# Optimization experiments

Hardware: AMD Instinct MI355X
Metric: run time of the kernel (lower is better)

Reference implementation:

```python
import jax, jax.numpy as jnp
import numpy as np
from jax import lax

# mamba-130m-hf config
N_LAYERS = 24
D_MODEL = 768
D_INNER = 1536   # expand=2
D_STATE = 16
DT_RANK = 48     # ceil(768/16)
D_CONV = 4
VOCAB = 50280
ENC_DIM = 256
EPS = 1e-5
SEQ, BATCH = 512, 2  # input is (SEQ, BATCH, ENC_DIM); permute -> mamba batch=BATCH, seq=SEQ


def setup_inputs() -> dict:
    key = jax.random.key(0)
    ks = jax.random.split(key, 12)
    f = jnp.float32
    def rn(k, shape, scale=0.02):
        return (jax.random.normal(k, shape) * scale).astype(f)
    x = jax.random.normal(ks[0], (SEQ, BATCH, ENC_DIM), dtype=f)
    W_et = rn(ks[1], (D_MODEL, ENC_DIM))
    b_et = jnp.zeros((D_MODEL,), f)
    in_proj_w = rn(ks[2], (N_LAYERS, 2 * D_INNER, D_MODEL))
    conv_w = rn(ks[3], (N_LAYERS, D_INNER, D_CONV), 0.1)
    conv_b = jnp.zeros((N_LAYERS, D_INNER), f)
    x_proj_w = rn(ks[4], (N_LAYERS, DT_RANK + 2 * D_STATE, D_INNER))
    dt_proj_w = rn(ks[5], (N_LAYERS, D_INNER, DT_RANK), 0.1)
    # bias init so softplus(bias) lands in [1e-3, 1e-1] (standard mamba dt init)
    dt_init = jnp.exp(jax.random.uniform(ks[6], (N_LAYERS, D_INNER), minval=jnp.log(1e-3), maxval=jnp.log(1e-1)))
    dt_proj_b = jnp.log(jnp.expm1(dt_init)).astype(f)
    A_log = jnp.log(jnp.broadcast_to(jnp.arange(1, D_STATE + 1, dtype=f), (N_LAYERS, D_INNER, D_STATE))) * jnp.ones((1,), f)
    D = jnp.ones((N_LAYERS, D_INNER), f)
    out_proj_w = rn(ks[7], (N_LAYERS, D_MODEL, D_INNER))
    norm_w = jnp.ones((N_LAYERS, D_MODEL), f)
    final_norm_w = jnp.ones((D_MODEL,), f)
    embed = rn(ks[8], (VOCAB, D_MODEL))
    return {"x": x, "W_et": W_et, "b_et": b_et, "in_proj_w": in_proj_w, "conv_w": conv_w,
            "conv_b": conv_b, "x_proj_w": x_proj_w, "dt_proj_w": dt_proj_w, "dt_proj_b": dt_proj_b,
            "A_log": A_log, "D": D, "out_proj_w": out_proj_w, "norm_w": norm_w,
            "final_norm_w": final_norm_w, "embed": embed}


def rmsnorm(x, w):
    return x * lax.rsqrt(jnp.mean(x * x, axis=-1, keepdims=True) + EPS) * w


def mamba_layer(h, p):
    in_w, cw, cb, xw, dtw, dtb, Al, Dv, ow, nw = p
    hn = rmsnorm(h, nw)
    xz = hn @ in_w.T                       # (B,T,2*D_INNER)
    xi, z = jnp.split(xz, 2, axis=-1)
    # depthwise causal conv over time
    xc = lax.conv_general_dilated(xi.transpose(0, 2, 1), cw[:, None, :], (1,),
                                  [(D_CONV - 1, 0)], dimension_numbers=("NCH", "OIH", "NCH"),
                                  feature_group_count=D_INNER)
    xc = jax.nn.silu(xc + cb[None, :, None]).transpose(0, 2, 1)   # (B,T,D_INNER)
    proj = xc @ xw.T                                              # (B,T,DT_RANK+2*D_STATE)
    dt = jax.nn.softplus(proj[..., :DT_RANK] @ dtw.T + dtb)       # (B,T,D_INNER)
    Bm = proj[..., DT_RANK:DT_RANK + D_STATE]                     # (B,T,S)
    Cm = proj[..., DT_RANK + D_STATE:]                            # (B,T,S)
    A = -jnp.exp(Al)                                              # (D_INNER,S)
    dA = jnp.exp(dt[..., None] * A)                               # (B,T,D,S)
    dBx = dt[..., None] * Bm[:, :, None, :] * xc[..., None]       # (B,T,D,S)

    def step(hst, inp):
        a, bx, c = inp
        hst = a * hst + bx
        return hst, jnp.einsum("bds,bs->bd", hst, c)

    h0 = jnp.zeros(dA.shape[:1] + dA.shape[2:], dA.dtype)
    _, ys = lax.scan(step, h0, (dA.transpose(1, 0, 2, 3), dBx.transpose(1, 0, 2, 3), Cm.transpose(1, 0, 2)))
    y = ys.transpose(1, 0, 2) + Dv * xc
    y = y * jax.nn.silu(z)
    return h + y @ ow.T


def reference(x, W_et, b_et, in_proj_w, conv_w, conv_b, x_proj_w, dt_proj_w, dt_proj_b,
              A_log, D, out_proj_w, norm_w, final_norm_w, embed):
    h = (x @ W_et.T + b_et).transpose(1, 0, 2)   # permute(1,0,2): (B,T,D_MODEL)

    def body(hc, p):
        return mamba_layer(hc, p), None

    h, _ = lax.scan(body, h, (in_proj_w, conv_w, conv_b, x_proj_w, dt_proj_w,
                              dt_proj_b, A_log, D, out_proj_w, norm_w))
    h = rmsnorm(h, final_norm_w)
    return h @ embed.T                            # tied lm_head logits (B,T,VOCAB)
```

## Files before the change

### kernel.cpp

```cpp
#include <hip/hip_runtime.h>
#include <math.h>

#define N_LAYERS 24
#define D_MODEL 768
#define D_INNER 1536
#define D_STATE 16
#define DT_RANK 48
#define D_CONV 4
#define VOCAB 50280
#define ENC_DIM 256
#define SEQ 512
#define BATCH 2
#define NTOK (SEQ*BATCH)
#define XZ_DIM (2*D_INNER)
#define PROJ_DIM (DT_RANK + 2*D_STATE)
#define DTW_PAD 64
#define IN_SPLIT 2
#define XP_SPLIT 8
#define OP_SPLIT 4

typedef __attribute__((ext_vector_type(8))) short bf16x8;
typedef __attribute__((ext_vector_type(4))) float f32x4;

__device__ __forceinline__ float sigmoidf_(float x) { return 1.f / (1.f + __expf(-x)); }
__device__ __forceinline__ float softplusf_(float x) {
    return fmaxf(x, 0.f) + log1pf(__expf(-fabsf(x)));
}
__device__ __forceinline__ short f2bf(float f) {
    unsigned u = __float_as_uint(f);
    unsigned r = (u + 0x7FFFu + ((u >> 16) & 1u)) >> 16;
    return (short)r;
}
__device__ __forceinline__ float bf2f(short s) {
    return __uint_as_float(((unsigned)(unsigned short)s) << 16);
}
__device__ __forceinline__ void load_lds16(const void* g, void* l) {
    __builtin_amdgcn_global_load_lds((const __attribute__((address_space(1))) void*)g,
                                     (__attribute__((address_space(3))) void*)l, 16, 0, 0);
}

__global__ __launch_bounds__(256) void cvt_k(const float* __restrict__ s,
                                             short* __restrict__ d, int n) {
    int stride = gridDim.x * 256 * 4;
    for (int i = (blockIdx.x * 256 + threadIdx.x) * 4; i + 3 < n; i += stride) {
        float4 f = *(const float4*)(s + i);
        short4 o; o.x = f2bf(f.x); o.y = f2bf(f.y); o.z = f2bf(f.z); o.w = f2bf(f.w);
        *(short4*)(d + i) = o;
    }
}

__global__ __launch_bounds__(256) void pad_dtw_k(const float* __restrict__ src,
                                                 short* __restrict__ dst) {
    int i = blockIdx.x * 256 + threadIdx.x;
    if (i >= N_LAYERS * D_INNER * DTW_PAD) return;
    int k = i & (DTW_PAD - 1);
    int rest = i >> 6;
    dst[i] = (k < DT_RANK) ? f2bf(src[(size_t)rest * DT_RANK + k]) : (short)0;
}

__global__ __launch_bounds__(256) void transpose_x_k(const float* __restrict__ x,
                                                     float* __restrict__ xt) {
    int i = blockIdx.x * 256 + threadIdx.x;
    if (i >= SEQ * BATCH * ENC_DIM) return;
    int e = i % ENC_DIM;
    int b = (i / ENC_DIM) % BATCH;
    int l = i / (ENC_DIM * BATCH);
    xt[((size_t)(b * SEQ + l)) * ENC_DIM + e] = x[i];
}
__global__ __launch_bounds__(256) void transpose_x_bf_k(const float* __restrict__ x,
                                                        short* __restrict__ xt) {
    int i = blockIdx.x * 256 + threadIdx.x;
    if (i >= SEQ * BATCH * ENC_DIM) return;
    int e = i % ENC_DIM;
    int b = (i / ENC_DIM) % BATCH;
    int l = i / (ENC_DIM * BATCH);
    xt[((size_t)(b * SEQ + l)) * ENC_DIM + e] = f2bf(x[i]);
}

__device__ __forceinline__ float rms_scale(const float* r, int tid) {
    float s = 0.f;
    for (int i = tid; i < D_MODEL; i += 256) { float v = r[i]; s += v * v; }
    for (int o = 32; o > 0; o >>= 1) s += __shfl_down(s, o);
    __shared__ float wsum[4];
    if ((tid & 63) == 0) wsum[tid >> 6] = s;
    __syncthreads();
    float tot = wsum[0] + wsum[1] + wsum[2] + wsum[3];
    return rsqrtf(tot / (float)D_MODEL + 1e-5f);
}
__global__ __launch_bounds__(256) void rmsnorm_k(const float* __restrict__ in,
                                                 const float* __restrict__ w,
                                                 float* __restrict__ out) {
    int row = blockIdx.x;
    const float* r = in + (size_t)row * D_MODEL;
    float sc = rms_scale(r, threadIdx.x);
    for (int i = threadIdx.x; i < D_MODEL; i += 256)
        out[(size_t)row * D_MODEL + i] = r[i] * sc * w[i];
}
__global__ __launch_bounds__(256) void rmsnorm_bf_k(const float* __restrict__ in,
                                                    const float* __restrict__ w,
                                                    short* __restrict__ out) {
    int row = blockIdx.x;
    const float* r = in + (size_t)row * D_MODEL;
    float sc = rms_scale(r, threadIdx.x);
    for (int i = threadIdx.x; i < D_MODEL; i += 256)
        out[(size_t)row * D_MODEL + i] = f2bf(r[i] * sc * w[i]);
}

template<int MODE, int BM, int DEPTH>
__global__ __launch_bounds__(256)
void gemm_p2(const short* __restrict__ A, const short* __restrict__ B,
             const float* __restrict__ bias, float* __restrict__ C,
             short* __restrict__ Cb,
             int M, int N, int K, int ldaE, int ldbE, int ldc, int ldcb)
{
    constexpr int NBUF = DEPTH + 1;
    constexpr int MI = BM / 32;
    constexpr int AELEM = 4 * BM;
    constexpr int BELEM = 4 * 128;
    constexpr int LA = AELEM / 256;
    constexpr int LB = BELEM / 256;
    constexpr int L = LA + LB;
    __shared__ short lA[NBUF][AELEM * 8];
    __shared__ short lB[NBUF][BELEM * 8];

    const int nx = gridDim.x;
    int lin = blockIdx.y * nx + blockIdx.x;
    const int nwg = nx * gridDim.y;
    if ((nwg & 7) == 0) { const int cpx = nwg >> 3; lin = (lin & 7) * cpx + (lin >> 3); }
    const int bm = (lin % nx) * BM;
    const int bn = (lin / nx) * 128;
    const int koff = blockIdx.z * K;

    const int t = threadIdx.x;
    const int wave = t >> 6;
    const int wm = (wave >> 1) * (BM / 2), wn = (wave & 1) * 64;
    const int l15 = t & 15, l4 = (t & 63) >> 4;

    f32x4 acc[MI][4] = {};
    const int nkt = K / 32;

    auto stage = [&](int buf, int kt) {
        const int k0 = koff + kt * 32;
        #pragma unroll
        for (int u = 0; u < LA; ++u) {
            const int idx = t + u * 256;
            const int kg = idx / BM;
            const int row = idx % BM;
            load_lds16(A + (size_t)(bm + row) * ldaE + k0 + kg * 8,
                       &lA[buf][(wave * 64 + u * 256) * 8]);
        }
        #pragma unroll
        for (int u = 0; u < LB; ++u) {
            const int idx = t + u * 256;
            const int kg = idx >> 7;
            const int row = idx & 127;
            int brow = bn + row; if (brow >= N) brow = 0;
            load_lds16(B + (size_t)brow * ldbE + k0 + kg * 8,
                       &lB[buf][(wave * 64 + u * 256) * 8]);
        }
    };

    #pragma unroll
    for (int p = 0; p < DEPTH; ++p)
        if (p < nkt) stage(p, p);

    for (int kt = 0; kt < nkt; ++kt) {
        const int rem = nkt - 1 - kt;
        const int ahead = rem < (DEPTH - 1) ? rem : (DEPTH - 1);
        if (ahead == 2) {
            if constexpr (L == 3) asm volatile("s_waitcnt vmcnt(6)" ::: "memory");
            else                  asm volatile("s_waitcnt vmcnt(8)" ::: "memory");
        } else if (ahead == 1) {
            if constexpr (L == 3) asm volatile("s_waitcnt vmcnt(3)" ::: "memory");
            else                  asm volatile("s_waitcnt vmcnt(4)" ::: "memory");
        } else {
            asm volatile("s_waitcnt vmcnt(0)" ::: "memory");
        }
        __builtin_amdgcn_s_barrier();
        __builtin_amdgcn_sched_barrier(0);
        if (kt + DEPTH < nkt) stage((kt + DEPTH) % NBUF, kt + DEPTH);
        const int cbuf = kt % NBUF;
        const short* bA = lA[cbuf];
        const short* bB = lB[cbuf];
        bf16x8 af[MI], bfr[4];
        #pragma unroll
        for (int i = 0; i < MI; ++i)
            af[i] = *(const bf16x8*)&bA[(l4 * BM + wm + i * 16 + l15) * 8];
        #pragma unroll
        for (int j = 0; j < 4; ++j)
            bfr[j] = *(const bf16x8*)&bB[(l4 * 128 + wn + j * 16 + l15) * 8];
        #pragma unroll
        for (int i = 0; i < MI; ++i)
            #pragma unroll
            for (int j = 0; j < 4; ++j)
                acc[i][j] = __builtin_amdgcn_mfma_f32_16x16x32_bf16(
                    af[i], bfr[j], acc[i][j], 0, 0, 0);
    }

    float* Cp = (MODE == 5) ? C + (size_t)blockIdx.z * M * ldc : C;
    #pragma unroll
    for (int i = 0; i < MI; ++i) {
        #pragma unroll
        for (int r = 0; r < 4; ++r) {
            const int row = bm + wm + i * 16 + l4 * 4 + r;
            #pragma unroll
            for (int j = 0; j < 4; ++j) {
                const int col = bn + wn + j * 16 + l15;
                if (col < N) {
                    float v = acc[i][j][r];
                    if (MODE == 6) {
                        Cb[(size_t)row * ldcb + col] = f2bf(softplusf_(v + bias[col]));
                    } else {
                        if (MODE == 1) v += bias[col];
                        if (MODE == 2) v = softplusf_(v + bias[col]);
                        if (MODE == 3) v += C[(size_t)row * ldc + col];
                        Cp[(size_t)row * ldc + col] = v;
                        if (MODE == 4) Cb[(size_t)row * ldcb + col] = f2bf(v);
                    }
                }
            }
        }
    }
}

__global__ __launch_bounds__(256) void reduce_conv_k(const float* __restrict__ part,
                                                     const float* __restrict__ cw,
                                                     const float* __restrict__ cb,
                                                     short* __restrict__ xcb,
                                                     short* __restrict__ zb) {
    int idx = blockIdx.x * 256 + threadIdx.x;
    if (idx >= NTOK * XZ_DIM) return;
    int d3 = idx % XZ_DIM;
    int m  = idx / XZ_DIM;
    if (d3 < D_INNER) {
        int l = m % SEQ;
        float acc = cb[d3];
        #pragma unroll
        for (int j = 0; j < D_CONV; ++j) {
            int ll = l - (D_CONV - 1) + j;
            if (ll >= 0) {
                int mm = m - (D_CONV - 1) + j;
                float v = part[(size_t)mm * XZ_DIM + d3]
                        + part[(size_t)(NTOK + mm) * XZ_DIM + d3];
                acc = fmaf(cw[d3 * D_CONV + j], v, acc);
            }
        }
        float v = acc * sigmoidf_(acc);
        xcb[(size_t)m * D_INNER + d3] = f2bf(v);
    } else {
        int d = d3 - D_INNER;
        float z = part[(size_t)m * XZ_DIM + d3]
                + part[(size_t)(NTOK + m) * XZ_DIM + d3];
        zb[(size_t)m * D_INNER + d] = f2bf(z);
    }
}

__global__ __launch_bounds__(256) void reduce_xp_k(const float* __restrict__ part,
                                                   float* __restrict__ proj,
                                                   short* __restrict__ projb) {
    const int n4 = NTOK * PROJ_DIM / 4;
    int i = blockIdx.x * 256 + threadIdx.x;
    if (i >= n4) return;
    float4 s = ((const float4*)part)[i];
    #pragma unroll
    for (int p = 1; p < XP_SPLIT; ++p) {
        float4 v = ((const float4*)part)[i + p * n4];
        s.x += v.x; s.y += v.y; s.z += v.z; s.w += v.w;
    }
    ((float4*)proj)[i] = s;
    short4 o; o.x = f2bf(s.x); o.y = f2bf(s.y); o.z = f2bf(s.z); o.w = f2bf(s.w);
    ((short4*)projb)[i] = o;
}

__global__ __launch_bounds__(256) void reduce_rms_k(const float* __restrict__ part,
                                                    float* __restrict__ h,
                                                    const float* __restrict__ w,
                                                    short* __restrict__ hnb) {
    const int row = blockIdx.x;
    const int i = threadIdx.x;
    float4 s = make_float4(0.f, 0.f, 0.f, 0.f);
    if (i < 192) {
        s = ((const float4*)h)[row * 192 + i];
        #pragma unroll
        for (int p = 0; p < OP_SPLIT; ++p) {
            float4 v = ((const float4*)part)[((size_t)p * NTOK + row) * 192 + i];
            s.x += v.x; s.y += v.y; s.z += v.z; s.w += v.w;
        }
        ((float4*)h)[row * 192 + i] = s;
    }
    float ss = s.x * s.x + s.y * s.y + s.z * s.z + s.w * s.w;
    for (int o = 32; o > 0; o >>= 1) ss += __shfl_down(ss, o);
    __shared__ float wsum[4];
    if ((i & 63) == 0) wsum[i >> 6] = ss;
    __syncthreads();
    float tot = wsum[0] + wsum[1] + wsum[2] + wsum[3];
    float sc = rsqrtf(tot / (float)D_MODEL + 1e-5f);
    if (i < 192) {
        float4 w4 = ((const float4*)w)[i];
        short4 o4;
        o4.x = f2bf(s.x * sc * w4.x); o4.y = f2bf(s.y * sc * w4.y);
        o4.z = f2bf(s.z * sc * w4.z); o4.w = f2bf(s.w * sc * w4.w);
        ((short4*)hnb)[row * 192 + i] = o4;
    }
}

template<int MODE>
__global__ __launch_bounds__(256)
void gemm_bf16(const float* __restrict__ A, const float* __restrict__ B,
               const float* __restrict__ bias, float* __restrict__ C,
               int M, int N, int K, int lda, int ldb, int ldc)
{
    __shared__ short lA[4 * 128 * 8];
    __shared__ short lB[4 * 128 * 8];
    const int bm = blockIdx.x * 128;
    const int bn = blockIdx.y * 128;
    const int t = threadIdx.x;
    const int wave = t >> 6, lane = t & 63;
    const int wm = (wave >> 1) * 64, wn = (wave & 1) * 64;
    const int l15 = lane & 15, l4 = lane >> 4;
    const int row2 = t >> 1;
    const int khalf = (t & 1) * 16;
    const int kgbase = khalf >> 3;
    f32x4 acc[4][4] = {};
    const int nkt = (K + 31) / 32;
    for (int kt = 0; kt < nkt; ++kt) {
        const int k0 = kt * 32 + khalf;
        {
            short v[16];
            const float* src = A + (size_t)(bm + row2) * lda + k0;
            if (k0 + 16 <= K) {
                #pragma unroll
                for (int j = 0; j < 16; j += 4) {
                    float4 f = *(const float4*)(src + j);
                    v[j+0]=f2bf(f.x); v[j+1]=f2bf(f.y); v[j+2]=f2bf(f.z); v[j+3]=f2bf(f.w);
                }
            } else {
                #pragma unroll
                for (int j = 0; j < 16; ++j)
                    v[j] = (k0 + j < K) ? f2bf(src[j]) : (short)0;
            }
            short* dst = &lA[(kgbase * 128 + row2) * 8];
            *(bf16x8*)dst = *(const bf16x8*)&v[0];
            *(bf16x8*)(dst + 128 * 8) = *(const bf16x8*)&v[8];
        }
        {
            short v[16];
            const int nrow = bn + row2;
            if (nrow < N) {
                const float* src = B + (size_t)nrow * ldb + k0;
                if (k0 + 16 <= K) {
                    #pragma unroll
                    for (int j = 0; j < 16; j += 4) {
                        float4 f = *(const float4*)(src + j);
                        v[j+0]=f2bf(f.x); v[j+1]=f2bf(f.y); v[j+2]=f2bf(f.z); v[j+3]=f2bf(f.w);
                    }
                } else {
                    #pragma unroll
                    for (int j = 0; j < 16; ++j)
                        v[j] = (k0 + j < K) ? f2bf(src[j]) : (short)0;
                }
            } else {
                #pragma unroll
                for (int j = 0; j < 16; ++j) v[j] = 0;
            }
            short* dst = &lB[(kgbase * 128 + row2) * 8];
            *(bf16x8*)dst = *(const bf16x8*)&v[0];
            *(bf16x8*)(dst + 128 * 8) = *(const bf16x8*)&v[8];
        }
        __syncthreads();
        bf16x8 af[4], bfr[4];
        #pragma unroll
        for (int i = 0; i < 4; ++i)
            af[i] = *(const bf16x8*)&lA[(l4 * 128 + wm + i * 16 + l15) * 8];
        #pragma unroll
        for (int j = 0; j < 4; ++j)
            bfr[j] = *(const bf16x8*)&lB[(l4 * 128 + wn + j * 16 + l15) * 8];
        #pragma unroll
        for (int i = 0; i < 4; ++i)
            #pragma unroll
            for (int j = 0; j < 4; ++j)
                acc[i][j] = __builtin_amdgcn_mfma_f32_16x16x32_bf16(
                    af[i], bfr[j], acc[i][j], 0, 0, 0);
        __syncthreads();
    }
    #pragma unroll
    for (int i = 0; i < 4; ++i) {
        #pragma unroll
        for (int r = 0; r < 4; ++r) {
            const int row = bm + wm + i * 16 + l4 * 4 + r;
            #pragma unroll
            for (int j = 0; j < 4; ++j) {
                const int col = bn + wn + j * 16 + l15;
                if (col < N) {
                    float v = acc[i][j][r];
                    if (MODE == 1) v += bias[col];
                    if (MODE == 2) v = softplusf_(v + bias[col]);
                    if (MODE == 3) v += C[(size_t)row * ldc + col];
                    C[(size_t)row * ldc + col] = v;
                }
            }
        }
    }
}

template<int DUAL>
__global__ __launch_bounds__(256) void conv_silu_k(const float* __restrict__ xz,
                                                   const float* __restrict__ cw,
                                                   const float* __restrict__ cb,
                                                   float* __restrict__ xc,
                                                   short* __restrict__ xcb) {
    int idx = blockIdx.x * 256 + threadIdx.x;
    if (idx >= NTOK * D_INNER) return;
    int d = idx % D_INNER;
    int m = idx / D_INNER;
    int l = m % SEQ;
    float acc = cb[d];
    #pragma unroll
    for (int j = 0; j < D_CONV; ++j) {
        int ll = l - (D_CONV - 1) + j;
        if (ll >= 0)
            acc = fmaf(cw[d * D_CONV + j],
                       xz[(size_t)(m - (D_CONV - 1) + j) * XZ_DIM + d], acc);
    }
    float v = acc * sigmoidf_(acc);
    xc[(size_t)m * D_INNER + d] = v;
    if (DUAL) xcb[(size_t)m * D_INNER + d] = f2bf(v);
}

#define SCAN_DW 16
#define SCAN_NC 32
#define SCAN_CL (SEQ / SCAN_NC)
template<int BF>
__global__ __launch_bounds__(512) void scan3_k(const float* __restrict__ proj,
                                               const void* __restrict__ dtp,
                                               const void* __restrict__ xcp,
                                               const void* __restrict__ zp,
                                               int zld,
                                               const float* __restrict__ A_log,
                                               const float* __restrict__ Dvec,
                                               void* __restrict__ yout) {
    __shared__ float lp[D_STATE][SCAN_NC][SCAN_DW];
    __shared__ float ls[D_STATE][SCAN_NC][SCAN_DW];
    const int nblk_d = D_INNER / SCAN_DW;
    const int b  = blockIdx.x / nblk_d;
    const int d0 = (blockIdx.x % nblk_d) * SCAN_DW;
    const int t  = threadIdx.x;
    const int dl = t & (SCAN_DW - 1);
    const int c  = t >> 4;
    const int d  = d0 + dl;

    float A[D_STATE];
    #pragma unroll
    for (int s = 0; s < D_STATE; s += 4) {
        float4 a4 = *(const float4*)&A_log[(size_t)d * D_STATE + s];
        A[s+0] = -__expf(a4.x); A[s+1] = -__expf(a4.y);
        A[s+2] = -__expf(a4.z); A[s+3] = -__expf(a4.w);
    }
    const int m0 = b * SEQ + c * SCAN_CL;

    float P[D_STATE], S[D_STATE];
    #pragma unroll
    for (int s = 0; s < D_STATE; ++s) { P[s] = 1.f; S[s] = 0.f; }
    for (int i = 0; i < SCAN_CL; ++i) {
        const int m = m0 + i;
        float dtv, xcv;
        if (BF) {
            dtv = bf2f(((const short*)dtp)[(size_t)m * D_INNER + d]);
            xcv = bf2f(((const short*)xcp)[(size_t)m * D_INNER + d]);
        } else {
            dtv = ((const float*)dtp)[(size_t)m * D_INNER + d];
            xcv = ((const float*)xcp)[(size_t)m * D_INNER + d];
        }
        float dx = dtv * xcv;
        const float* pB = proj + (size_t)m * PROJ_DIM + DT_RANK;
        float Bv[D_STATE];
        #pragma unroll
        for (int s = 0; s < D_STATE; s += 4)
            *(float4*)&Bv[s] = *(const float4*)(pB + s);
        #pragma unroll
        for (int s = 0; s < D_STATE; ++s) {
            float da = __expf(dtv * A[s]);
            S[s] = fmaf(da, S[s], dx * Bv[s]);
            P[s] *= da;
        }
    }
    #pragma unroll
    for (int s = 0; s < D_STATE; ++s) { lp[s][c][dl] = P[s]; ls[s][c][dl] = S[s]; }
    __syncthreads();

    float st[D_STATE];
    #pragma unroll
    for (int s = 0; s < D_STATE; ++s) st[s] = 0.f;
    for (int j = 0; j < c; ++j) {
        #pragma unroll
        for (int s = 0; s < D_STATE; ++s)
            st[s] = fmaf(lp[s][j][dl], st[s], ls[s][j][dl]);
    }

    const float Dvv = Dvec[d];
    for (int i = 0; i < SCAN_CL; ++i) {
        const int m = m0 + i;
        float dtv, xcv, zv;
        if (BF) {
            dtv = bf2f(((const short*)dtp)[(size_t)m * D_INNER + d]);
            xcv = bf2f(((const short*)xcp)[(size_t)m * D_INNER + d]);
            zv  = bf2f(((const short*)zp)[(size_t)m * zld + d]);
        } else {
            dtv = ((const float*)dtp)[(size_t)m * D_INNER + d];
            xcv = ((const float*)xcp)[(size_t)m * D_INNER + d];
            zv  = ((const float*)zp)[(size_t)m * zld + d];
        }
        float dx = dtv * xcv;
        const float* pB = proj + (size_t)m * PROJ_DIM + DT_RANK;
        float Bv[D_STATE], Cv[D_STATE];
        #pragma unroll
        for (int s = 0; s < D_STATE; s += 4) {
            *(float4*)&Bv[s] = *(const float4*)(pB + s);
            *(float4*)&Cv[s] = *(const float4*)(pB + D_STATE + s);
        }
        float acc = Dvv * xcv;
        #pragma unroll
        for (int s = 0; s < D_STATE; ++s) {
            float da = __expf(dtv * A[s]);
            st[s] = fmaf(da, st[s], dx * Bv[s]);
            acc = fmaf(st[s], Cv[s], acc);
        }
        float yv = acc * (zv * sigmoidf_(zv));
        if (BF) ((short*)yout)[(size_t)m * D_INNER + d] = f2bf(yv);
        else    ((float*)yout)[(size_t)m * D_INNER + d] = yv;
    }
}

extern "C" void kernel_launch(void* const* d_in, const int* in_sizes, int n_in,
                              void* d_out, int out_size, void* d_ws, size_t ws_size,
                              hipStream_t stream) {
    const float* x           = (const float*)d_in[0];
    const float* W_et        = (const float*)d_in[1];
    const float* b_et        = (const float*)d_in[2];
    const float* in_proj_w   = (const float*)d_in[3];
    const float* conv_w      = (const float*)d_in[4];
    const float* conv_b      = (const float*)d_in[5];
    const float* x_proj_w    = (const float*)d_in[6];
    const float* dt_proj_w   = (const float*)d_in[7];
    const float* dt_proj_b   = (const float*)d_in[8];
    const float* A_log       = (const float*)d_in[9];
    const float* Dv          = (const float*)d_in[10];
    const float* out_proj_w  = (const float*)d_in[11];
    const float* norm_w      = (const float*)d_in[12];
    const float* final_norm_w= (const float*)d_in[13];
    const float* embed       = (const float*)d_in[14];
    float* out = (float*)d_out;
    float* ws  = (float*)d_ws;

    float* h       = ws;
    float* proj    = h + (size_t)NTOK * D_MODEL;
    float* scratch = proj + (size_t)NTOK * PROJ_DIM;
    short* xt_bf   = (short*)(scratch + (size_t)IN_SPLIT * NTOK * XZ_DIM);
    short* hn_bf   = xt_bf   + (size_t)NTOK * ENC_DIM;
    short* xc_bf   = hn_bf   + (size_t)NTOK * D_MODEL;
    short* z_bf    = xc_bf   + (size_t)NTOK * D_INNER;
    short* dt_bf   = z_bf    + (size_t)NTOK * D_INNER;
    short* proj_bf = dt_bf   + (size_t)NTOK * D_INNER;
    short* yb_bf   = proj_bf + (size_t)NTOK * PROJ_DIM;
    short* wet_bf  = yb_bf   + (size_t)NTOK * D_INNER;
    short* inw_bf  = wet_bf  + (size_t)D_MODEL * ENC_DIM;
    short* xw_bf   = inw_bf  + (size_t)N_LAYERS * XZ_DIM * D_MODEL;
    short* dtw_bf  = xw_bf   + (size_t)N_LAYERS * PROJ_DIM * D_INNER;
    short* ow_bf   = dtw_bf  + (size_t)N_LAYERS * D_INNER * DTW_PAD;
    short* emb_bf  = ow_bf   + (size_t)N_LAYERS * D_MODEL * D_INNER;
    short* end_bf  = emb_bf  + (size_t)VOCAB * D_MODEL;
    size_t needA = (size_t)((char*)end_bf - (char*)d_ws);
    bool tierA = ws_size >= needA;

    dim3 blk(256);
    const int scan_blocks = BATCH * (D_INNER / SCAN_DW);

    if (tierA) {
        auto cvt = [&](const float* s, short* d, size_t n) {
            int nb = (int)((n / 4 + 255) / 256); if (nb > 2048) nb = 2048;
            cvt_k<<<nb, blk, 0, stream>>>(s, d, (int)n);
        };
        cvt(W_et, wet_bf, (size_t)D_MODEL * ENC_DIM);
        cvt(in_proj_w, inw_bf, (size_t)N_LAYERS * XZ_DIM * D_MODEL);
        cvt(x_proj_w, xw_bf, (size_t)N_LAYERS * PROJ_DIM * D_INNER);
        cvt(out_proj_w, ow_bf, (size_t)N_LAYERS * D_MODEL * D_INNER);
        cvt(embed, emb_bf, (size_t)VOCAB * D_MODEL);
        pad_dtw_k<<<(N_LAYERS * D_INNER * DTW_PAD + 255) / 256, blk, 0, stream>>>(
            dt_proj_w, dtw_bf);

        transpose_x_bf_k<<<(SEQ * BATCH * ENC_DIM + 255) / 256, blk, 0, stream>>>(x, xt_bf);
        gemm_p2<1, 64, 2><<<dim3(NTOK / 64, D_MODEL / 128), blk, 0, stream>>>(
            xt_bf, wet_bf, b_et, h, nullptr,
            NTOK, D_MODEL, ENC_DIM, ENC_DIM, ENC_DIM, D_MODEL, 0);
        rmsnorm_bf_k<<<NTOK, blk, 0, stream>>>(h, norm_w, hn_bf);

        for (int L = 0; L < N_LAYERS; ++L) {
            const short* in_w = inw_bf + (size_t)L * XZ_DIM * D_MODEL;
            const float* cw   = conv_w + (size_t)L * D_INNER * D_CONV;
            const float* cb   = conv_b + (size_t)L * D_INNER;
            const short* xw   = xw_bf  + (size_t)L * PROJ_DIM * D_INNER;
            const short* dtw  = dtw_bf + (size_t)L * D_INNER * DTW_PAD;
            const float* dtbp = dt_proj_b + (size_t)L * D_INNER;
            const float* Al   = A_log  + (size_t)L * D_INNER * D_STATE;
            const float* Dl   = Dv     + (size_t)L * D_INNER;
            const short* ow   = ow_bf  + (size_t)L * D_MODEL * D_INNER;
            const float* nw_next = (L == N_LAYERS - 1) ? final_norm_w
                                 : norm_w + (size_t)(L + 1) * D_MODEL;

            gemm_p2<5, 64, 3><<<dim3(NTOK / 64, XZ_DIM / 128, IN_SPLIT), blk, 0, stream>>>(
                hn_bf, in_w, nullptr, scratch, nullptr,
                NTOK, XZ_DIM, D_MODEL / IN_SPLIT, D_MODEL, D_MODEL, XZ_DIM, 0);
            reduce_conv_k<<<(NTOK * XZ_DIM + 255) / 256, blk, 0, stream>>>(
                scratch, cw, cb, xc_bf, z_bf);
            gemm_p2<5, 64, 3><<<dim3(NTOK / 64, 1, XP_SPLIT), blk, 0, stream>>>(
                xc_bf, xw, nullptr, scratch, nullptr,
                NTOK, PROJ_DIM, D_INNER / XP_SPLIT, D_INNER, D_INNER, PROJ_DIM, 0);
            reduce_xp_k<<<(NTOK * PROJ_DIM / 4 + 255) / 256, blk, 0, stream>>>(
                scratch, proj, proj_bf);
            gemm_p2<6, 64, 2><<<dim3(NTOK / 64, D_INNER / 128), blk, 0, stream>>>(
                proj_bf, dtw, dtbp, h , dt_bf,
                NTOK, D_INNER, DTW_PAD, PROJ_DIM, DTW_PAD, D_INNER, D_INNER);
            scan3_k<1><<<scan_blocks, dim3(512), 0, stream>>>(
                proj, dt_bf, xc_bf, z_bf, D_INNER, Al, Dl, yb_bf);
            gemm_p2<5, 64, 3><<<dim3(NTOK / 64, D_MODEL / 128, OP_SPLIT), blk, 0, stream>>>(
                yb_bf, ow, nullptr, scratch, nullptr,
                NTOK, D_MODEL, D_INNER / OP_SPLIT, D_INNER, D_INNER, D_MODEL, 0);
            reduce_rms_k<<<NTOK, blk, 0, stream>>>(scratch, h, nw_next, hn_bf);
        }

        gemm_p2<0, 128, 2><<<dim3(NTOK / 128, (VOCAB + 127) / 128), blk, 0, stream>>>(
            hn_bf, emb_bf, nullptr, out, nullptr,
            NTOK, VOCAB, D_MODEL, D_MODEL, D_MODEL, VOCAB, 0);
    } else {
        float* hB   = ws;
        float* hnB  = hB   + (size_t)NTOK * D_MODEL;
        float* xzB  = hnB  + (size_t)NTOK * D_MODEL;
        float* xcB  = xzB  + (size_t)NTOK * XZ_DIM;
        float* projB= xcB  + (size_t)NTOK * D_INNER;
        float* dtB  = projB+ (size_t)NTOK * PROJ_DIM;
        float* ybB  = dtB  + (size_t)NTOK * D_INNER;

        transpose_x_k<<<(SEQ * BATCH * ENC_DIM + 255) / 256, blk, 0, stream>>>(x, ybB);
        gemm_bf16<1><<<dim3(NTOK / 128, D_MODEL / 128), blk, 0, stream>>>(
            ybB, W_et, b_et, hB, NTOK, D_MODEL, ENC_DIM, ENC_DIM, ENC_DIM, D_MODEL);
        for (int L = 0; L < N_LAYERS; ++L) {
            const float* in_w = in_proj_w  + (size_t)L * XZ_DIM * D_MODEL;
            const float* cw   = conv_w     + (size_t)L * D_INNER * D_CONV;
            const float* cb   = conv_b     + (size_t)L * D_INNER;
            const float* xw   = x_proj_w   + (size_t)L * PROJ_DIM * D_INNER;
            const float* dtw  = dt_proj_w  + (size_t)L * D_INNER * DT_RANK;
            const float* dtbp = dt_proj_b  + (size_t)L * D_INNER;
            const float* Al   = A_log      + (size_t)L * D_INNER * D_STATE;
            const float* Dl   = Dv         + (size_t)L * D_INNER;
            const float* ow   = out_proj_w + (size_t)L * D_MODEL * D_INNER;
            const float* nw   = norm_w     + (size_t)L * D_MODEL;
            rmsnorm_k<<<NTOK, blk, 0, stream>>>(hB, nw, hnB);
            gemm_bf16<0><<<dim3(NTOK / 128, XZ_DIM / 128), blk, 0, stream>>>(
                hnB, in_w, nullptr, xzB, NTOK, XZ_DIM, D_MODEL, D_MODEL, D_MODEL, XZ_DIM);
            conv_silu_k<0><<<(NTOK * D_INNER + 255) / 256, blk, 0, stream>>>(
                xzB, cw, cb, xcB, nullptr);
            gemm_bf16<0><<<dim3(NTOK / 128, 1), blk, 0, stream>>>(
                xcB, xw, nullptr, projB, NTOK, PROJ_DIM, D_INNER, D_INNER, D_INNER, PROJ_DIM);
            gemm_bf16<2><<<dim3(NTOK / 128, D_INNER / 128), blk, 0, stream>>>(
                projB, dtw, dtbp, dtB, NTOK, D_INNER, DT_RANK, PROJ_DIM, DT_RANK, D_INNER);
            scan3_k<0><<<scan_blocks, dim3(512), 0, stream>>>(
                projB, dtB, xcB, xzB + D_INNER, XZ_DIM, Al, Dl, ybB);
            gemm_bf16<3><<<dim3(NTOK / 128, D_MODEL / 128), blk, 0, stream>>>(
                ybB, ow, nullptr, hB, NTOK, D_MODEL, D_INNER, D_INNER, D_INNER, D_MODEL);
        }
        rmsnorm_k<<<NTOK, blk, 0, stream>>>(hB, final_norm_w, hnB);
        gemm_bf16<0><<<dim3(NTOK / 128, (VOCAB + 127) / 128), blk, 0, stream>>>(
            hnB, embed, nullptr, out, NTOK, VOCAB, D_MODEL, D_MODEL, D_MODEL, VOCAB);
    }
}
```

Before: 3.011 ms.

## Store split-K GEMM partials in bf16 and balance XCD block remapping

Adds a GEMM epilogue mode that writes split-K partial sums as bf16 rather than fp32. The in_proj, x_proj and out_proj reductions now read these bf16 partials, which halves scratch traffic between each GEMM and its reduce kernel. The XCD-aware block index remap is generalised to grids whose block count is not a multiple of 8, and the vmcnt waits move into a template helper. The cost is rounding partial sums to bf16 before accumulation, which lowers accuracy, including on the residual stream update.

```diff
diff --git a/kernel.cpp b/kernel.cpp
--- a/kernel.cpp
+++ b/kernel.cpp
@@ -38,6 +38,15 @@
     __builtin_amdgcn_global_load_lds((const __attribute__((address_space(1))) void*)g,
                                      (__attribute__((address_space(3))) void*)l, 16, 0, 0);
 }
+template<int V> __device__ __forceinline__ void vwait() {
+    if constexpr (V == 0)       asm volatile("s_waitcnt vmcnt(0)" ::: "memory");
+    else if constexpr (V == 3)  asm volatile("s_waitcnt vmcnt(3)" ::: "memory");
+    else if constexpr (V == 4)  asm volatile("s_waitcnt vmcnt(4)" ::: "memory");
+    else if constexpr (V == 6)  asm volatile("s_waitcnt vmcnt(6)" ::: "memory");
+    else if constexpr (V == 8)  asm volatile("s_waitcnt vmcnt(8)" ::: "memory");
+    else if constexpr (V == 12) asm volatile("s_waitcnt vmcnt(12)" ::: "memory");
+    else                        asm volatile("s_waitcnt vmcnt(0)" ::: "memory");
+}
 
 __global__ __launch_bounds__(256) void cvt_k(const float* __restrict__ s,
                                              short* __restrict__ d, int n) {
@@ -126,7 +135,11 @@
     const int nx = gridDim.x;
     int lin = blockIdx.y * nx + blockIdx.x;
     const int nwg = nx * gridDim.y;
-    if ((nwg & 7) == 0) { const int cpx = nwg >> 3; lin = (lin & 7) * cpx + (lin >> 3); }
+    {
+        const int q = nwg >> 3, r = nwg & 7;
+        const int xcd = lin & 7, win = lin >> 3;
+        lin = (xcd < r ? xcd * (q + 1) : r * (q + 1) + (xcd - r) * q) + win;
+    }
     const int bm = (lin % nx) * BM;
     const int bn = (lin / nx) * 128;
     const int koff = blockIdx.z * K;
@@ -167,15 +180,9 @@
     for (int kt = 0; kt < nkt; ++kt) {
         const int rem = nkt - 1 - kt;
         const int ahead = rem < (DEPTH - 1) ? rem : (DEPTH - 1);
-        if (ahead == 2) {
-            if constexpr (L == 3) asm volatile("s_waitcnt vmcnt(6)" ::: "memory");
-            else                  asm volatile("s_waitcnt vmcnt(8)" ::: "memory");
-        } else if (ahead == 1) {
-            if constexpr (L == 3) asm volatile("s_waitcnt vmcnt(3)" ::: "memory");
-            else                  asm volatile("s_waitcnt vmcnt(4)" ::: "memory");
-        } else {
-            asm volatile("s_waitcnt vmcnt(0)" ::: "memory");
-        }
+        if (ahead == 2)      vwait<2 * L>();
+        else if (ahead == 1) vwait<L>();
+        else                 vwait<0>();
         __builtin_amdgcn_s_barrier();
         __builtin_amdgcn_sched_barrier(0);
         if (kt + DEPTH < nkt) stage((kt + DEPTH) % NBUF, kt + DEPTH);
@@ -198,6 +205,7 @@
     }
 
     float* Cp = (MODE == 5) ? C + (size_t)blockIdx.z * M * ldc : C;
+    short* Cbp = (MODE == 7) ? Cb + (size_t)blockIdx.z * M * ldcb : Cb;
     #pragma unroll
     for (int i = 0; i < MI; ++i) {
         #pragma unroll
@@ -210,6 +218,8 @@
                     float v = acc[i][j][r];
                     if (MODE == 6) {
                         Cb[(size_t)row * ldcb + col] = f2bf(softplusf_(v + bias[col]));
+                    } else if (MODE == 7) {
+                        Cbp[(size_t)row * ldcb + col] = f2bf(v);
                     } else {
                         if (MODE == 1) v += bias[col];
                         if (MODE == 2) v = softplusf_(v + bias[col]);
@@ -223,7 +233,7 @@
     }
 }
 
-__global__ __launch_bounds__(256) void reduce_conv_k(const float* __restrict__ part,
+__global__ __launch_bounds__(256) void reduce_conv_k(const short* __restrict__ part,
                                                      const float* __restrict__ cw,
                                                      const float* __restrict__ cb,
                                                      short* __restrict__ xcb,
@@ -240,8 +250,8 @@
             int ll = l - (D_CONV - 1) + j;
             if (ll >= 0) {
                 int mm = m - (D_CONV - 1) + j;
-                float v = part[(size_t)mm * XZ_DIM + d3]
-                        + part[(size_t)(NTOK + mm) * XZ_DIM + d3];
+                float v = bf2f(part[(size_t)mm * XZ_DIM + d3])
+                        + bf2f(part[(size_t)(NTOK + mm) * XZ_DIM + d3]);
                 acc = fmaf(cw[d3 * D_CONV + j], v, acc);
             }
         }
@@ -249,30 +259,31 @@
         xcb[(size_t)m * D_INNER + d3] = f2bf(v);
     } else {
         int d = d3 - D_INNER;
-        float z = part[(size_t)m * XZ_DIM + d3]
-                + part[(size_t)(NTOK + m) * XZ_DIM + d3];
+        float z = bf2f(part[(size_t)m * XZ_DIM + d3])
+                + bf2f(part[(size_t)(NTOK + m) * XZ_DIM + d3]);
         zb[(size_t)m * D_INNER + d] = f2bf(z);
     }
 }
 
-__global__ __launch_bounds__(256) void reduce_xp_k(const float* __restrict__ part,
+__global__ __launch_bounds__(256) void reduce_xp_k(const short* __restrict__ part,
                                                    float* __restrict__ proj,
                                                    short* __restrict__ projb) {
     const int n4 = NTOK * PROJ_DIM / 4;
     int i = blockIdx.x * 256 + threadIdx.x;
     if (i >= n4) return;
-    float4 s = ((const float4*)part)[i];
-    #pragma unroll
-    for (int p = 1; p < XP_SPLIT; ++p) {
-        float4 v = ((const float4*)part)[i + p * n4];
-        s.x += v.x; s.y += v.y; s.z += v.z; s.w += v.w;
-    }
+    float sx = 0.f, sy = 0.f, sz = 0.f, sw = 0.f;
+    #pragma unroll
+    for (int p = 0; p < XP_SPLIT; ++p) {
+        short4 v = ((const short4*)part)[i + p * n4];
+        sx += bf2f(v.x); sy += bf2f(v.y); sz += bf2f(v.z); sw += bf2f(v.w);
+    }
+    float4 s = make_float4(sx, sy, sz, sw);
     ((float4*)proj)[i] = s;
-    short4 o; o.x = f2bf(s.x); o.y = f2bf(s.y); o.z = f2bf(s.z); o.w = f2bf(s.w);
+    short4 o; o.x = f2bf(sx); o.y = f2bf(sy); o.z = f2bf(sz); o.w = f2bf(sw);
     ((short4*)projb)[i] = o;
 }
 
-__global__ __launch_bounds__(256) void reduce_rms_k(const float* __restrict__ part,
+__global__ __launch_bounds__(256) void reduce_rms_k(const short* __restrict__ part,
                                                     float* __restrict__ h,
                                                     const float* __restrict__ w,
                                                     short* __restrict__ hnb) {
@@ -283,8 +294,8 @@
         s = ((const float4*)h)[row * 192 + i];
         #pragma unroll
         for (int p = 0; p < OP_SPLIT; ++p) {
-            float4 v = ((const float4*)part)[((size_t)p * NTOK + row) * 192 + i];
-            s.x += v.x; s.y += v.y; s.z += v.z; s.w += v.w;
+            short4 v = ((const short4*)part)[((size_t)p * NTOK + row) * 192 + i];
+            s.x += bf2f(v.x); s.y += bf2f(v.y); s.z += bf2f(v.z); s.w += bf2f(v.w);
         }
         ((float4*)h)[row * 192 + i] = s;
     }
@@ -555,6 +566,7 @@
     float* h       = ws;
     float* proj    = h + (size_t)NTOK * D_MODEL;
     float* scratch = proj + (size_t)NTOK * PROJ_DIM;
+    short* scratch_bf = (short*)scratch;
     short* xt_bf   = (short*)(scratch + (size_t)IN_SPLIT * NTOK * XZ_DIM);
     short* hn_bf   = xt_bf   + (size_t)NTOK * ENC_DIM;
     short* xc_bf   = hn_bf   + (size_t)NTOK * D_MODEL;
@@ -607,25 +619,25 @@
             const float* nw_next = (L == N_LAYERS - 1) ? final_norm_w
                                  : norm_w + (size_t)(L + 1) * D_MODEL;
 
-            gemm_p2<5, 64, 3><<<dim3(NTOK / 64, XZ_DIM / 128, IN_SPLIT), blk, 0, stream>>>(
-                hn_bf, in_w, nullptr, scratch, nullptr,
-                NTOK, XZ_DIM, D_MODEL / IN_SPLIT, D_MODEL, D_MODEL, XZ_DIM, 0);
+            gemm_p2<7, 64, 3><<<dim3(NTOK / 64, XZ_DIM / 128, IN_SPLIT), blk, 0, stream>>>(
+                hn_bf, in_w, nullptr, nullptr, scratch_bf,
+                NTOK, XZ_DIM, D_MODEL / IN_SPLIT, D_MODEL, D_MODEL, 0, XZ_DIM);
             reduce_conv_k<<<(NTOK * XZ_DIM + 255) / 256, blk, 0, stream>>>(
-                scratch, cw, cb, xc_bf, z_bf);
-            gemm_p2<5, 64, 3><<<dim3(NTOK / 64, 1, XP_SPLIT), blk, 0, stream>>>(
-                xc_bf, xw, nullptr, scratch, nullptr,
-                NTOK, PROJ_DIM, D_INNER / XP_SPLIT, D_INNER, D_INNER, PROJ_DIM, 0);
+                scratch_bf, cw, cb, xc_bf, z_bf);
+            gemm_p2<7, 64, 3><<<dim3(NTOK / 64, 1, XP_SPLIT), blk, 0, stream>>>(
+                xc_bf, xw, nullptr, nullptr, scratch_bf,
+                NTOK, PROJ_DIM, D_INNER / XP_SPLIT, D_INNER, D_INNER, 0, PROJ_DIM);
             reduce_xp_k<<<(NTOK * PROJ_DIM / 4 + 255) / 256, blk, 0, stream>>>(
-                scratch, proj, proj_bf);
+                scratch_bf, proj, proj_bf);
             gemm_p2<6, 64, 2><<<dim3(NTOK / 64, D_INNER / 128), blk, 0, stream>>>(
                 proj_bf, dtw, dtbp, h , dt_bf,
                 NTOK, D_INNER, DTW_PAD, PROJ_DIM, DTW_PAD, D_INNER, D_INNER);
             scan3_k<1><<<scan_blocks, dim3(512), 0, stream>>>(
                 proj, dt_bf, xc_bf, z_bf, D_INNER, Al, Dl, yb_bf);
-            gemm_p2<5, 64, 3><<<dim3(NTOK / 64, D_MODEL / 128, OP_SPLIT), blk, 0, stream>>>(
-                yb_bf, ow, nullptr, scratch, nullptr,
-                NTOK, D_MODEL, D_INNER / OP_SPLIT, D_INNER, D_INNER, D_MODEL, 0);
-            reduce_rms_k<<<NTOK, blk, 0, stream>>>(scratch, h, nw_next, hn_bf);
+            gemm_p2<7, 64, 3><<<dim3(NTOK / 64, D_MODEL / 128, OP_SPLIT), blk, 0, stream>>>(
+                yb_bf, ow, nullptr, nullptr, scratch_bf,
+                NTOK, D_MODEL, D_INNER / OP_SPLIT, D_INNER, D_INNER, 0, D_MODEL);
+            reduce_rms_k<<<NTOK, blk, 0, stream>>>(scratch_bf, h, nw_next, hn_bf);
         }
 
         gemm_p2<0, 128, 2><<<dim3(NTOK / 128, (VOCAB + 127) / 128), blk, 0, stream>>>(
```

Result: no change. 2.981 ms (-1.0%).
